# Kernel optimization log

Hardware: AMD Instinct MI355X
Metric: run time of the kernel (lower is better)

Reference implementation:

```python
import jax, jax.numpy as jnp
import numpy as np

B, DIM, Hs, Ws_ = 16, 96, 112, 112
HEADS, WS, OUT = 3, 7, 96
DH = OUT // HEADS


def _rel_index(ws):
    ch = np.arange(ws)
    coords = np.stack(np.meshgrid(ch, ch, indexing='ij'), 0).reshape(2, -1)
    rel = (coords[:, :, None] - coords[:, None, :]).transpose(1, 2, 0).copy()
    rel[..., 0] += ws - 1
    rel[..., 1] += ws - 1
    rel[..., 0] *= 2 * ws - 1
    return rel.sum(-1)  # [ws*ws, ws*ws]


def grid_sample_zeros(img, grid):
    # img [N,C,H,W], grid [N,Hg,Wg,2] with (x,y) in [-1,1]; bilinear, align_corners=True, zeros padding
    N, C, H, W = img.shape
    x = (grid[..., 0] + 1.0) * 0.5 * (W - 1)
    y = (grid[..., 1] + 1.0) * 0.5 * (H - 1)
    x0 = jnp.floor(x); y0 = jnp.floor(y)
    x1 = x0 + 1.0; y1 = y0 + 1.0
    wa = (x1 - x) * (y1 - y); wb = (x - x0) * (y1 - y)
    wc = (x1 - x) * (y - y0); wd = (x - x0) * (y - y0)

    def gather(ix, iy):
        valid = ((ix >= 0) & (ix <= W - 1) & (iy >= 0) & (iy <= H - 1)).astype(img.dtype)
        ixc = jnp.clip(ix, 0, W - 1).astype(jnp.int32)
        iyc = jnp.clip(iy, 0, H - 1).astype(jnp.int32)
        vals = jax.vmap(lambda im, yy, xx: im[:, yy, xx])(img, iyc, ixc)  # [N,C,Hg,Wg]
        return vals * valid[:, None, :, :]

    return (gather(x0, y0) * wa[:, None] + gather(x1, y0) * wb[:, None]
            + gather(x0, y1) * wc[:, None] + gather(x1, y1) * wd[:, None])


def setup_inputs() -> dict:
    key = jax.random.key(0)
    ks = jax.random.split(key, 8)
    s = 0.02
    return {
        'x': jax.random.normal(ks[0], (B, DIM, Hs, Ws_), jnp.float32),
        'w_qkv': jax.random.normal(ks[1], (3 * OUT, DIM), jnp.float32) * s,
        'b_qkv': jnp.zeros((3 * OUT,), jnp.float32),
        'w_off': jax.random.normal(ks[2], (2 * HEADS, DIM), jnp.float32) * s,
        'b_off': jnp.zeros((2 * HEADS,), jnp.float32),
        'w_scl': jax.random.normal(ks[3], (2 * HEADS, DIM), jnp.float32) * s,
        'b_scl': jnp.zeros((2 * HEADS,), jnp.float32),
        'rpb': jax.random.normal(ks[4], ((2 * WS - 1) ** 2, HEADS), jnp.float32) * s,
        'w_proj': jax.random.normal(ks[5], (OUT, OUT), jnp.float32) * s,
        'b_proj': jnp.zeros((OUT,), jnp.float32),
    }


def _forward(x, w_qkv, b_qkv, w_off, b_off, w_scl, b_scl, rpb, w_proj, b_proj):
    b, C, h, w = x.shape
    ws, H, dh = WS, HEADS, DH
    scale = (C // H) ** -0.5
    pad_td = (ws - h % ws) % ws; pad_lr = (ws - w % ws) % ws
    pt, pd = pad_td // 2, pad_td - pad_td // 2
    pl, pr = pad_lr // 2, pad_lr - pad_lr // 2
    eh, ew = h + pad_td, w + pad_lr
    wnh, wnw = eh // ws, ew // ws
    xp = jnp.pad(x, ((0, 0), (0, 0), (pt, pd), (pl, pr)))

    # base reference grid, channel 0 = x (width), channel 1 = y (height)
    irh = jnp.linspace(-1.0, 1.0, eh); irw = jnp.linspace(-1.0, 1.0, ew)
    base = jnp.stack([jnp.broadcast_to(irw[None, :], (eh, ew)),
                      jnp.broadcast_to(irh[:, None], (eh, ew))], 0).reshape(2, wnh, ws, wnw, ws)
    bch = jnp.arange(ws) * 2.0 / (eh - 1); bch = bch - bch.mean()
    bcw = jnp.arange(ws) * 2.0 / (ew - 1); bcw = bcw - bcw.mean()
    wc = jnp.stack([jnp.broadcast_to(bcw[None, None, None, :], (wnh, ws, wnw, ws)),
                    jnp.broadcast_to(bch[None, :, None, None], (wnh, ws, wnw, ws))], 0)

    # per-window offset / scale prediction: avgpool(ws) -> leaky_relu -> 1x1 conv
    pooled = xp.reshape(b, C, wnh, ws, wnw, ws).mean(axis=(3, 5))
    act = jax.nn.leaky_relu(pooled)  # slope 0.01, matches torch default
    off = (jnp.einsum('bchw,oc->bohw', act, w_off) + b_off[None, :, None, None]).reshape(b * H, 2, wnh, wnw)
    off = jnp.stack([off[:, 0] / (h // ws), off[:, 1] / (w // ws)], 1)
    scl = (jnp.einsum('bchw,oc->bohw', act, w_scl) + b_scl[None, :, None, None]).reshape(b * H, 2, wnh, wnw)

    coords = base[None] + wc[None] * scl[:, :, :, None, :, None] + off[:, :, :, None, :, None]
    grid = coords.transpose(0, 2, 3, 4, 5, 1).reshape(b * H, eh, ew, 2)

    qkv = jnp.einsum('bchw,oc->bohw', x, w_qkv) + b_qkv[None, :, None, None]
    qkv = qkv.reshape(b, 3, H, dh, h, w).transpose(1, 0, 2, 3, 4, 5).reshape(3 * b * H, dh, h, w)
    qkv = jnp.pad(qkv, ((0, 0), (0, 0), (pt, pd), (pl, pr))).reshape(3, b * H, dh, eh, ew)
    q, k, v = qkv[0], qkv[1], qkv[2]

    k_s = grid_sample_zeros(k, grid)
    v_s = grid_sample_zeros(v, grid)

    def to_win(t):  # [b*H, dh, eh, ew] -> [b*wnh*wnw, H, ws*ws, dh]
        return t.reshape(b, H, dh, wnh, ws, wnw, ws).transpose(0, 3, 5, 1, 4, 6, 2).reshape(b * wnh * wnw, H, ws * ws, dh)

    qw, kw, vw = to_win(q), to_win(k_s), to_win(v_s)
    dots = jnp.einsum('wnqd,wnkd->wnqk', qw, kw) * scale
    rel_idx = jnp.asarray(_rel_index(ws))
    bias = rpb[rel_idx.reshape(-1)].reshape(ws * ws, ws * ws, H).transpose(2, 0, 1)
    attn = jax.nn.softmax(dots + bias[None], axis=-1)
    out = jnp.einsum('wnqk,wnkd->wnqd', attn, vw)
    out = out.reshape(b, wnh, wnw, H, ws, ws, dh).transpose(0, 3, 6, 1, 4, 2, 5).reshape(b, H * dh, eh, ew)
    out = out[:, :, pt:h + pt, pl:w + pl]
    out = jnp.einsum('bchw,oc->bohw', out, w_proj) + b_proj[None, :, None, None]
    return out


def reference(x, w_qkv, b_qkv, w_off, b_off, w_scl, b_scl, rpb, w_proj, b_proj):
    return _forward(x, w_qkv, b_qkv, w_off, b_off, w_scl, b_scl, rpb, w_proj, b_proj)
```

## Files before the change

### kernel.cpp

```cpp
#include <hip/hip_runtime.h>
#include <hip/hip_bf16.h>
#include <stdint.h>

#define NB 16
#define CDIM 96
#define HW 112
#define NPOS (HW*HW)
#define NHEAD 3
#define DH 32
#define WN 16
#define NWIN (WN*WN)
#define SCALE 0.17677669529663687f

typedef __attribute__((ext_vector_type(8))) short bf16x8;
typedef __attribute__((ext_vector_type(4))) float f32x4;

__device__ __forceinline__ float bfbits_lo(uint32_t w){ union{uint32_t u; float f;} a; a.u = w<<16; return a.f; }
__device__ __forceinline__ float bfbits_hi(uint32_t w){ union{uint32_t u; float f;} a; a.u = w & 0xFFFF0000u; return a.f; }
__device__ __forceinline__ uint32_t packbf(float x, float y){
  union{float f; uint32_t u;} a, b; a.f = x; b.f = y;
  uint32_t ua = a.u + 0x7FFFu + ((a.u>>16)&1u);
  uint32_t ub = b.u + 0x7FFFu + ((b.u>>16)&1u);
  return (ua>>16) | (ub & 0xFFFF0000u);
}
__device__ __forceinline__ unsigned short f2bf(float x){
  union{float f; uint32_t u;} a; a.f = x;
  return (unsigned short)((a.u + 0x7FFFu + ((a.u>>16)&1u))>>16);
}

__global__ void k_pool_act(const float* __restrict__ x, float* __restrict__ act){
  int n = blockIdx.x*256 + threadIdx.x;
  int ww = n & 15; int wh = (n>>4)&15; int bc = n>>8;
  const float* src = x + (size_t)bc*NPOS + (size_t)(wh*7)*HW + ww*7;
  float s = 0.f;
  #pragma unroll
  for (int r=0;r<7;r++){
    const float* row = src + r*HW;
    s += row[0]+row[1]+row[2]+row[3]+row[4]+row[5]+row[6];
  }
  s *= (1.f/49.f);
  act[n] = s > 0.f ? s : 0.01f*s;
}

__global__ void k_offscl(const float* __restrict__ act,
                         const float* __restrict__ woff, const float* __restrict__ boff,
                         const float* __restrict__ wscl, const float* __restrict__ bscl,
                         float4* __restrict__ offscl){
  int n = blockIdx.x*256 + threadIdx.x;
  int b = n >> 8; int wpos = n & 255;
  float accO[6], accS[6];
  #pragma unroll
  for (int o=0;o<6;o++){ accO[o]=boff[o]; accS[o]=bscl[o]; }
  const float* a = act + (size_t)b*CDIM*NWIN + wpos;
  for (int c=0;c<CDIM;c++){
    float av = a[(size_t)c*NWIN];
    #pragma unroll
    for (int o=0;o<6;o++){ accO[o] += av*woff[o*CDIM+c]; accS[o] += av*wscl[o*CDIM+c]; }
  }
  #pragma unroll
  for (int h=0;h<NHEAD;h++){
    float4 r;
    r.x = accO[2*h]   * (1.f/16.f);
    r.y = accO[2*h+1] * (1.f/16.f);
    r.z = accS[2*h];
    r.w = accS[2*h+1];
    offscl[(size_t)(b*NHEAD+h)*NWIN + wpos] = r;
  }
}

__global__ void k_bias_pre(const float* __restrict__ rpb, float* __restrict__ bias_g){
  int n = blockIdx.x*256 + threadIdx.x;
  if (n >= 3*64*64) return;
  int h = n >> 12; int q = (n>>6)&63; int k = n&63;
  float v = -1e30f;
  if (k < 49){
    int qc = q < 49 ? q : 48;
    int qi = qc/7, qj = qc - (qc/7)*7;
    int ki = k/7,  kj = k - (k/7)*7;
    v = rpb[((qi-ki+6)*13 + (qj-kj+6))*3 + h];
  }
  bias_g[n] = v;
}

__launch_bounds__(256)
__global__ void k_qkv_mfma(const float* __restrict__ x, const float* __restrict__ wqkv,
                           const float* __restrict__ bqkv,
                           unsigned short* __restrict__ q, unsigned short* __restrict__ kk,
                           unsigned short* __restrict__ v){
  __shared__ float xf[96*72];
  __shared__ uint4 xbf4[64*13];
  __shared__ uint4 wbf4[96*13];
  const int t = threadIdx.x;
  const int b = blockIdx.x / 196;
  const int p0 = (blockIdx.x % 196) * 64;

  #pragma unroll
  for (int i=0;i<6;i++){
    int f = t + i*256; int c = f>>4; int p4 = (f&15)*4;
    *(float4*)(xf + c*72 + p4) = *(const float4*)(x + (size_t)(b*CDIM+c)*NPOS + p0 + p4);
  }
  __syncthreads();
  #pragma unroll
  for (int i=0;i<3;i++){
    int u = t + i*256; int pos = u & 63; int oct = u >> 6;
    uint32_t pk0 = packbf(xf[(oct*8+0)*72+pos], xf[(oct*8+1)*72+pos]);
    uint32_t pk1 = packbf(xf[(oct*8+2)*72+pos], xf[(oct*8+3)*72+pos]);
    uint32_t pk2 = packbf(xf[(oct*8+4)*72+pos], xf[(oct*8+5)*72+pos]);
    uint32_t pk3 = packbf(xf[(oct*8+6)*72+pos], xf[(oct*8+7)*72+pos]);
    xbf4[pos*13 + oct] = make_uint4(pk0,pk1,pk2,pk3);
  }

  const int lane = t & 63, wv = t >> 6;
  const int g = lane >> 4, r16 = lane & 15;

  for (int s=0;s<3;s++){
    if (s) __syncthreads();
    #pragma unroll
    for (int i=0;i<9;i++){
      int f = t + i*256; int o = f/24; int c4m = f%24;
      float4 wvv = *(const float4*)(wqkv + (size_t)(s*96+o)*CDIM + c4m*4);
      ((uint2*)wbf4)[o*26 + c4m] = make_uint2(packbf(wvv.x,wvv.y), packbf(wvv.z,wvv.w));
    }
    __syncthreads();

    f32x4 acc[6];
    #pragma unroll
    for (int nf=0;nf<6;nf++) acc[nf] = (f32x4){0.f,0.f,0.f,0.f};
    #pragma unroll
    for (int ks=0;ks<3;ks++){
      bf16x8 a = *(const bf16x8*)&xbf4[(wv*16 + r16)*13 + ks*4 + g];
      #pragma unroll
      for (int nf=0;nf<6;nf++){
        bf16x8 bb = *(const bf16x8*)&wbf4[(nf*16 + r16)*13 + ks*4 + g];
        acc[nf] = __builtin_amdgcn_mfma_f32_16x16x32_bf16(a, bb, acc[nf], 0,0,0);
      }
    }
    unsigned short* dst = (s==0)?q:((s==1)?kk:v);
    float sc = (s==0) ? SCALE : 1.f;
    #pragma unroll
    for (int nf=0;nf<6;nf++){
      int o = nf*16 + r16; int h = o>>5; int d = o&31;
      float bv = bqkv[s*96+o];
      size_t base = ((size_t)(b*NHEAD+h)*NPOS + p0 + wv*16 + g*4)*DH + d;
      #pragma unroll
      for (int rr=0;rr<4;rr++)
        dst[base + (size_t)rr*DH] = f2bf((acc[nf][rr] + bv)*sc);
    }
  }
}

__device__ __forceinline__ void load_row_fma(const uint32_t* __restrict__ src, float w, float* acc){
  const uint4* p4 = (const uint4*)src;
  #pragma unroll
  for (int r=0;r<4;r++){
    uint4 u = p4[r];
    acc[r*8+0] += w*bfbits_lo(u.x); acc[r*8+1] += w*bfbits_hi(u.x);
    acc[r*8+2] += w*bfbits_lo(u.y); acc[r*8+3] += w*bfbits_hi(u.y);
    acc[r*8+4] += w*bfbits_lo(u.z); acc[r*8+5] += w*bfbits_hi(u.z);
    acc[r*8+6] += w*bfbits_lo(u.w); acc[r*8+7] += w*bfbits_hi(u.w);
  }
}

__launch_bounds__(128)
__global__ void k_attn_mfma(const unsigned short* __restrict__ qb,
                            const unsigned short* __restrict__ kb,
                            const unsigned short* __restrict__ vb,
                            const float4* __restrict__ offscl,
                            const float* __restrict__ bias_g,
                            float* __restrict__ aout){
  __shared__ unsigned short lds_u[2*8192];
  const int h   = blockIdx.x % 3;
  const int grp = blockIdx.x / 3;
  const int wv  = threadIdx.x >> 6;
  const int lane = threadIdx.x & 63;
  const int win = grp*2 + wv;
  const int b = win>>8, wh=(win>>4)&15, ww=win&15;
  const int bh = b*NHEAD + h;
  const int g = lane>>4, r16 = lane&15;

  unsigned short* K_s  = lds_u + wv*8192;
  unsigned short* VT_s = lds_u + wv*8192 + 2048;
  unsigned short* P_s  = lds_u + wv*8192 + 4096;

  uint4 qf[4];
  #pragma unroll
  for (int qt=0;qt<4;qt++){
    int qq = qt*16 + r16; if (qq > 48) qq = 48;
    int qi = qq/7; int qj = qq - qi*7;
    size_t pos = (size_t)(wh*7+qi)*HW + ww*7 + qj;
    qf[qt] = *(const uint4*)(qb + ((size_t)bh*NPOS + pos)*DH + g*8);
  }

  float krow[32], vrow[32];
  #pragma unroll
  for (int d=0;d<32;d++){ krow[d]=0.f; vrow[d]=0.f; }
  if (lane < 49){
    float4 os = offscl[(size_t)bh*NWIN + (wh*16+ww)];
    int ki = lane/7; int kj = lane - ki*7;
    float px = (float)(ww*7+kj) + (float)(kj-3)*os.z + 55.5f*os.x;
    float py = (float)(wh*7+ki) + (float)(ki-3)*os.w + 55.5f*os.y;
    float x0f = floorf(px), y0f = floorf(py);
    float fx = px-x0f, fy = py-y0f;
    int x0 = (int)x0f, y0 = (int)y0f;
    float wts[4] = {(1.f-fx)*(1.f-fy), fx*(1.f-fy), (1.f-fx)*fy, fx*fy};
    #pragma unroll
    for (int nb=0; nb<4; nb++){
      int xi = x0 + (nb&1);
      int yi = y0 + ((nb>>1)&1);
      if (xi>=0 && xi<HW && yi>=0 && yi<HW){
        size_t base = ((size_t)bh*NPOS + (size_t)yi*HW + xi)*DH;
        load_row_fma((const uint32_t*)(kb + base), wts[nb], krow);
        load_row_fma((const uint32_t*)(vb + base), wts[nb], vrow);
      }
    }
  }
  #pragma unroll
  for (int c16=0;c16<4;c16++){
    uint4 pk = make_uint4(packbf(krow[c16*8+0],krow[c16*8+1]), packbf(krow[c16*8+2],krow[c16*8+3]),
                          packbf(krow[c16*8+4],krow[c16*8+5]), packbf(krow[c16*8+6],krow[c16*8+7]));
    *(uint4*)&K_s[lane*32 + ((c16 ^ (lane&3))*8)] = pk;
  }
  #pragma unroll
  for (int d=0;d<32;d++){
    VT_s[d*64 + (((lane>>3) ^ (d&7))*8) + (lane&7)] = f2bf(vrow[d]);
  }

  const float* bias_h = bias_g + h*4096;
  f32x4 acc[4][4];
  #pragma unroll
  for (int qt=0;qt<4;qt++){
    int qq = qt*16 + r16;
    #pragma unroll
    for (int at=0;at<4;at++)
      acc[at][qt] = *(const f32x4*)(bias_h + qq*64 + at*16 + g*4);
  }
  #pragma unroll
  for (int at=0;at<4;at++){
    bf16x8 a = *(const bf16x8*)&K_s[(at*16+r16)*32 + ((g ^ (r16&3))*8)];
    #pragma unroll
    for (int qt=0;qt<4;qt++)
      acc[at][qt] = __builtin_amdgcn_mfma_f32_16x16x32_bf16(a, *(const bf16x8*)&qf[qt], acc[at][qt], 0,0,0);
  }

  #pragma unroll
  for (int qt=0;qt<4;qt++){
    float m = acc[0][qt][0];
    #pragma unroll
    for (int at=0;at<4;at++)
      #pragma unroll
      for (int rr=0;rr<4;rr++) m = fmaxf(m, acc[at][qt][rr]);
    m = fmaxf(m, __shfl_xor(m, 16));
    m = fmaxf(m, __shfl_xor(m, 32));
    float s = 0.f;
    #pragma unroll
    for (int at=0;at<4;at++)
      #pragma unroll
      for (int rr=0;rr<4;rr++){ float e = __expf(acc[at][qt][rr]-m); acc[at][qt][rr]=e; s+=e; }
    s += __shfl_xor(s, 16);
    s += __shfl_xor(s, 32);
    float rl = 1.f/s;
    #pragma unroll
    for (int at=0;at<4;at++)
      #pragma unroll
      for (int rr=0;rr<4;rr++) acc[at][qt][rr] *= rl;
  }

  #pragma unroll
  for (int qt=0;qt<4;qt++){
    int qq = qt*16 + r16;
    #pragma unroll
    for (int at=0;at<4;at++){
      uint2 pk = make_uint2(packbf(acc[at][qt][0], acc[at][qt][1]),
                            packbf(acc[at][qt][2], acc[at][qt][3]));
      *(uint2*)&P_s[qq*64 + (((2*at + (g>>1)) ^ (qq&7))*8) + 4*(g&1)] = pk;
    }
  }

  f32x4 o[4][2];
  #pragma unroll
  for (int mt=0;mt<4;mt++){ o[mt][0]=(f32x4){0,0,0,0}; o[mt][1]=(f32x4){0,0,0,0}; }
  #pragma unroll
  for (int kt=0;kt<2;kt++){
    bf16x8 bfr[2];
    #pragma unroll
    for (int nt=0;nt<2;nt++){
      int dh = nt*16 + r16;
      bfr[nt] = *(const bf16x8*)&VT_s[dh*64 + (((4*kt+g) ^ (r16&7))*8)];
    }
    #pragma unroll
    for (int mt=0;mt<4;mt++){
      int qq = mt*16 + r16;
      bf16x8 a = *(const bf16x8*)&P_s[qq*64 + (((4*kt+g) ^ (r16&7))*8)];
      o[mt][0] = __builtin_amdgcn_mfma_f32_16x16x32_bf16(a, bfr[0], o[mt][0], 0,0,0);
      o[mt][1] = __builtin_amdgcn_mfma_f32_16x16x32_bf16(a, bfr[1], o[mt][1], 0,0,0);
    }
  }

  float* outbase = aout + ((size_t)b*CDIM + h*DH)*NPOS;
  #pragma unroll
  for (int mt=0;mt<4;mt++){
    #pragma unroll
    for (int rr=0;rr<4;rr++){
      int qq = mt*16 + 4*g + rr;
      if (qq < 49){
        int qi = qq/7; int qj = qq - qi*7;
        size_t sp = (size_t)(wh*7+qi)*HW + ww*7 + qj;
        outbase[(size_t)r16*NPOS + sp]      = o[mt][0][rr];
        outbase[(size_t)(16+r16)*NPOS + sp] = o[mt][1][rr];
      }
    }
  }
}

__launch_bounds__(256)
__global__ void k_proj_mfma(const float* yin, const float* __restrict__ wproj,
                            const float* __restrict__ bproj, float* yout){
  __shared__ float xf[96*72];
  __shared__ uint4 xbf4[64*13];
  __shared__ uint4 wbf4[96*13];
  const int t = threadIdx.x;
  const int b = blockIdx.x / 196;
  const int p0 = (blockIdx.x % 196) * 64;

  #pragma unroll
  for (int i=0;i<6;i++){
    int f = t + i*256; int c = f>>4; int p4 = (f&15)*4;
    *(float4*)(xf + c*72 + p4) = *(const float4*)(yin + (size_t)(b*CDIM+c)*NPOS + p0 + p4);
  }
  __syncthreads();
  #pragma unroll
  for (int i=0;i<3;i++){
    int u = t + i*256; int pos = u & 63; int oct = u >> 6;
    uint32_t pk0 = packbf(xf[(oct*8+0)*72+pos], xf[(oct*8+1)*72+pos]);
    uint32_t pk1 = packbf(xf[(oct*8+2)*72+pos], xf[(oct*8+3)*72+pos]);
    uint32_t pk2 = packbf(xf[(oct*8+4)*72+pos], xf[(oct*8+5)*72+pos]);
    uint32_t pk3 = packbf(xf[(oct*8+6)*72+pos], xf[(oct*8+7)*72+pos]);
    xbf4[pos*13 + oct] = make_uint4(pk0,pk1,pk2,pk3);
  }
  #pragma unroll
  for (int i=0;i<9;i++){
    int f = t + i*256; int o = f/24; int c4m = f%24;
    float4 wvv = *(const float4*)(wproj + (size_t)o*CDIM + c4m*4);
    ((uint2*)wbf4)[o*26 + c4m] = make_uint2(packbf(wvv.x,wvv.y), packbf(wvv.z,wvv.w));
  }
  __syncthreads();

  const int lane = t & 63, wv = t >> 6;
  const int g = lane >> 4, r16 = lane & 15;
  f32x4 acc[6];
  #pragma unroll
  for (int nf=0;nf<6;nf++) acc[nf] = (f32x4){0.f,0.f,0.f,0.f};
  #pragma unroll
  for (int ks=0;ks<3;ks++){
    bf16x8 a = *(const bf16x8*)&xbf4[(wv*16 + r16)*13 + ks*4 + g];
    #pragma unroll
    for (int nf=0;nf<6;nf++){
      bf16x8 bb = *(const bf16x8*)&wbf4[(nf*16 + r16)*13 + ks*4 + g];
      acc[nf] = __builtin_amdgcn_mfma_f32_16x16x32_bf16(a, bb, acc[nf], 0,0,0);
    }
  }
  #pragma unroll
  for (int nf=0;nf<6;nf++){
    int o = nf*16 + r16;
    float bv = bproj[o];
    float* dst = yout + (size_t)(b*CDIM+o)*NPOS + p0 + wv*16 + g*4;
    #pragma unroll
    for (int rr=0;rr<4;rr++) dst[rr] = acc[nf][rr] + bv;
  }
}

extern "C" void kernel_launch(void* const* d_in, const int* in_sizes, int n_in,
                              void* d_out, int out_size, void* d_ws, size_t ws_size,
                              hipStream_t stream) {
  const float* x      = (const float*)d_in[0];
  const float* w_qkv  = (const float*)d_in[1];
  const float* b_qkv  = (const float*)d_in[2];
  const float* w_off  = (const float*)d_in[3];
  const float* b_off  = (const float*)d_in[4];
  const float* w_scl  = (const float*)d_in[5];
  const float* b_scl  = (const float*)d_in[6];
  const float* rpb    = (const float*)d_in[7];
  const float* w_proj = (const float*)d_in[8];
  const float* b_proj = (const float*)d_in[9];

  char* ws = (char*)d_ws;
  float*   act    = (float*)(ws + 0);
  float4*  offscl = (float4*)(ws + 1572864);
  float*   bias_g = (float*)(ws + 1769472);
  const size_t QKV_BYTES = (size_t)NB*NHEAD*NPOS*DH*2;
  unsigned short* qbuf = (unsigned short*)(ws + 2097152);
  unsigned short* kbuf = (unsigned short*)(ws + 2097152 + QKV_BYTES);
  unsigned short* vbuf = (unsigned short*)(ws + 2097152 + 2*QKV_BYTES);

  hipLaunchKernelGGL(k_pool_act,  dim3(1536), dim3(256), 0, stream, x, act);
  hipLaunchKernelGGL(k_offscl,    dim3(16),   dim3(256), 0, stream, act, w_off, b_off, w_scl, b_scl, offscl);
  hipLaunchKernelGGL(k_bias_pre,  dim3(48),   dim3(256), 0, stream, rpb, bias_g);
  hipLaunchKernelGGL(k_qkv_mfma,  dim3(16*196), dim3(256), 0, stream, x, w_qkv, b_qkv, qbuf, kbuf, vbuf);
  hipLaunchKernelGGL(k_attn_mfma, dim3(3*2048), dim3(128), 0, stream,
                     qbuf, kbuf, vbuf, offscl, bias_g, (float*)d_out);
  hipLaunchKernelGGL(k_proj_mfma, dim3(16*196), dim3(256), 0, stream,
                     (const float*)d_out, w_proj, b_proj, (float*)d_out);
}
```

Before: 225.8 us.

## Spread bilinear K/V gather across all lanes using shuffled neighbor addresses

The deformable K/V bilinear gather is redistributed. Before, 49 lanes each loaded full 64-byte rows (divergent, with 15 lanes idle). Now each lane computes clamped neighbor addresses and masked weights, these are broadcast with shuffles, and every lane loads a 16-byte slice for 4 sample positions. The intent is more coalesced, branch-free loads and shorter per-lane register chains. The cost is extra shuffles and added block-wide __syncthreads before the LDS reads.

```diff
diff --git a/kernel.cpp b/kernel.cpp
--- a/kernel.cpp
+++ b/kernel.cpp
@@ -146,18 +146,6 @@
       for (int rr=0;rr<4;rr++)
         dst[base + (size_t)rr*DH] = f2bf((acc[nf][rr] + bv)*sc);
     }
-  }
-}
-
-__device__ __forceinline__ void load_row_fma(const uint32_t* __restrict__ src, float w, float* acc){
-  const uint4* p4 = (const uint4*)src;
-  #pragma unroll
-  for (int r=0;r<4;r++){
-    uint4 u = p4[r];
-    acc[r*8+0] += w*bfbits_lo(u.x); acc[r*8+1] += w*bfbits_hi(u.x);
-    acc[r*8+2] += w*bfbits_lo(u.y); acc[r*8+3] += w*bfbits_hi(u.y);
-    acc[r*8+4] += w*bfbits_lo(u.z); acc[r*8+5] += w*bfbits_hi(u.z);
-    acc[r*8+6] += w*bfbits_lo(u.w); acc[r*8+7] += w*bfbits_hi(u.w);
   }
 }
 
@@ -191,39 +179,60 @@
     qf[qt] = *(const uint4*)(qb + ((size_t)bh*NPOS + pos)*DH + g*8);
   }
 
-  float krow[32], vrow[32];
-  #pragma unroll
-  for (int d=0;d<32;d++){ krow[d]=0.f; vrow[d]=0.f; }
-  if (lane < 49){
+  int ki = lane/7; int kj = lane - ki*7;
+  uint32_t nbaddr[4]; float nbw[4];
+  {
     float4 os = offscl[(size_t)bh*NWIN + (wh*16+ww)];
-    int ki = lane/7; int kj = lane - ki*7;
     float px = (float)(ww*7+kj) + (float)(kj-3)*os.z + 55.5f*os.x;
     float py = (float)(wh*7+ki) + (float)(ki-3)*os.w + 55.5f*os.y;
     float x0f = floorf(px), y0f = floorf(py);
     float fx = px-x0f, fy = py-y0f;
     int x0 = (int)x0f, y0 = (int)y0f;
-    float wts[4] = {(1.f-fx)*(1.f-fy), fx*(1.f-fy), (1.f-fx)*fy, fx*fy};
-    #pragma unroll
-    for (int nb=0; nb<4; nb++){
-      int xi = x0 + (nb&1);
-      int yi = y0 + ((nb>>1)&1);
-      if (xi>=0 && xi<HW && yi>=0 && yi<HW){
-        size_t base = ((size_t)bh*NPOS + (size_t)yi*HW + xi)*DH;
-        load_row_fma((const uint32_t*)(kb + base), wts[nb], krow);
-        load_row_fma((const uint32_t*)(vb + base), wts[nb], vrow);
-      }
-    }
-  }
-  #pragma unroll
-  for (int c16=0;c16<4;c16++){
-    uint4 pk = make_uint4(packbf(krow[c16*8+0],krow[c16*8+1]), packbf(krow[c16*8+2],krow[c16*8+3]),
-                          packbf(krow[c16*8+4],krow[c16*8+5]), packbf(krow[c16*8+6],krow[c16*8+7]));
-    *(uint4*)&K_s[lane*32 + ((c16 ^ (lane&3))*8)] = pk;
-  }
-  #pragma unroll
-  for (int d=0;d<32;d++){
-    VT_s[d*64 + (((lane>>3) ^ (d&7))*8) + (lane&7)] = f2bf(vrow[d]);
-  }
+    float wb[4] = {(1.f-fx)*(1.f-fy), fx*(1.f-fy), (1.f-fx)*fy, fx*fy};
+    bool qok = lane < 49;
+    #pragma unroll
+    for (int nb=0;nb<4;nb++){
+      int xi = x0 + (nb&1), yi = y0 + (nb>>1);
+      int xc = min(max(xi,0),HW-1), yc = min(max(yi,0),HW-1);
+      nbaddr[nb] = (uint32_t)(yc*HW + xc) * 64u;
+      nbw[nb] = (qok && xi==xc && yi==yc) ? wb[nb] : 0.f;
+    }
+  }
+
+  const char* kb8 = (const char*)kb + (size_t)bh*NPOS*64;
+  const char* vb8 = (const char*)vb + (size_t)bh*NPOS*64;
+  #pragma unroll
+  for (int pp=0;pp<4;pp++){
+    int spos = pp*16 + r16;
+    float ka[8], va[8];
+    #pragma unroll
+    for (int j=0;j<8;j++){ ka[j]=0.f; va[j]=0.f; }
+    #pragma unroll
+    for (int nb=0;nb<4;nb++){
+      uint32_t a = (uint32_t)__shfl((int)nbaddr[nb], spos);
+      float    w = __shfl(nbw[nb], spos);
+      uint4 uk = *(const uint4*)(kb8 + a + g*16);
+      uint4 uv = *(const uint4*)(vb8 + a + g*16);
+      ka[0]+=w*bfbits_lo(uk.x); ka[1]+=w*bfbits_hi(uk.x);
+      ka[2]+=w*bfbits_lo(uk.y); ka[3]+=w*bfbits_hi(uk.y);
+      ka[4]+=w*bfbits_lo(uk.z); ka[5]+=w*bfbits_hi(uk.z);
+      ka[6]+=w*bfbits_lo(uk.w); ka[7]+=w*bfbits_hi(uk.w);
+      va[0]+=w*bfbits_lo(uv.x); va[1]+=w*bfbits_hi(uv.x);
+      va[2]+=w*bfbits_lo(uv.y); va[3]+=w*bfbits_hi(uv.y);
+      va[4]+=w*bfbits_lo(uv.z); va[5]+=w*bfbits_hi(uv.z);
+      va[6]+=w*bfbits_lo(uv.w); va[7]+=w*bfbits_hi(uv.w);
+    }
+    uint4 pk = make_uint4(packbf(ka[0],ka[1]), packbf(ka[2],ka[3]),
+                          packbf(ka[4],ka[5]), packbf(ka[6],ka[7]));
+    *(uint4*)&K_s[spos*32 + ((g ^ (spos&3))*8)] = pk;
+    #pragma unroll
+    for (int j=0;j<8;j++){
+      int d = g*8 + j;
+      VT_s[d*64 + (((spos>>3) ^ (d&7))*8) + (spos&7)] = f2bf(va[j]);
+    }
+  }
+
+  __syncthreads();
 
   const float* bias_h = bias_g + h*4096;
   f32x4 acc[4][4];
@@ -275,6 +284,8 @@
       *(uint2*)&P_s[qq*64 + (((2*at + (g>>1)) ^ (qq&7))*8) + 4*(g&1)] = pk;
     }
   }
+
+  __syncthreads();
 
   f32x4 o[4][2];
   #pragma unroll
```

Result: slower. 242.4 us (+7.4%).
